# Kernel tuning notes

Measured on AMD Instinct MI355X. Metric: run time of the kernel, lower is better.

The kernel has to match this reference:

```python
import jax, jax.numpy as jnp
import numpy as np

B, L, H, V = 64, 2048, 1024, 50257


def setup_inputs() -> dict:
    key = jax.random.key(0)
    ks = jax.random.split(key, 12)
    s = 0.02
    return {
        "input_seq": jax.random.randint(ks[0], (B,), 0, V),
        "encoder_outputs": jax.random.normal(ks[1], (L, B, H), jnp.float32),
        "h0": jax.random.normal(ks[2], (1, B, H), jnp.float32),
        "c0": jax.random.normal(ks[3], (1, B, H), jnp.float32),
        "emb": jax.random.normal(ks[4], (V, H), jnp.float32) * s,
        "W_ih": jax.random.normal(ks[5], (4 * H, H), jnp.float32) * s,
        "W_hh": jax.random.normal(ks[6], (4 * H, H), jnp.float32) * s,
        "b_ih": jnp.zeros((4 * H,), jnp.float32),
        "b_hh": jnp.zeros((4 * H,), jnp.float32),
        "W_concat": jax.random.normal(ks[7], (H, 2 * H), jnp.float32) * s,
        "b_concat": jnp.zeros((H,), jnp.float32),
        "W_out": jax.random.normal(ks[8], (V, H), jnp.float32) * s,
        "b_out": jnp.zeros((V,), jnp.float32),
    }


def reference(input_seq, encoder_outputs, h0, c0, emb, W_ih, W_hh, b_ih, b_hh,
              W_concat, b_concat, W_out, b_out):
    # Embedding lookup (dropout is identity at eval)
    x = emb[input_seq]                      # [B, H]
    h, c = h0[0], c0[0]                     # [B, H] each (n_layers == 1)

    # Single LSTM step, PyTorch gate order (i, f, g, o)
    gates = x @ W_ih.T + b_ih + h @ W_hh.T + b_hh   # [B, 4H]
    i, f, g, o = jnp.split(gates, 4, axis=-1)
    i, f, o = jax.nn.sigmoid(i), jax.nn.sigmoid(f), jax.nn.sigmoid(o)
    g = jnp.tanh(g)
    c1 = f * c + i * g
    h1 = o * jnp.tanh(c1)                   # rnn_output, [B, H]

    # Luong 'dot' attention: replaces the per-(b,i) python double loop
    energies = jnp.einsum('bh,lbh->bl', h1, encoder_outputs)   # [B, L]
    attn = jax.nn.softmax(energies, axis=1)                    # [B, L]
    context = jnp.einsum('bl,lbh->bh', attn, encoder_outputs)  # [B, H]

    concat_out = jnp.tanh(jnp.concatenate([h1, context], axis=1) @ W_concat.T + b_concat)
    output = concat_out @ W_out.T + b_out                      # [B, V]

    return output, h1[None], c1[None], attn[:, None, :]
```

## Files before the change

kernel.cpp:

```cpp
#include <hip/hip_runtime.h>
#include <math.h>

#define B 64
#define Lw 2048
#define Hd 1024
#define Vd 50257

#define WS_CATB   0
#define WS_ENERGY 65536
#define WS_PART   196608
#define WS_CONC   2310144

#define OUT_H1   3216448
#define OUT_C1   3281984
#define OUT_ATTN 3347520

#define NCHUNK 32
#define LCHUNK 64
#define PSTRIDE 1032

typedef __bf16 bf16x8 __attribute__((ext_vector_type(8)));
typedef float f32x4 __attribute__((ext_vector_type(4)));

__device__ __forceinline__ float sigm(float x) { return 1.f / (1.f + expf(-x)); }

#define CVT8(dst, w0, w1)                                            \
    dst[0] = (__bf16)w0.x; dst[1] = (__bf16)w0.y;                    \
    dst[2] = (__bf16)w0.z; dst[3] = (__bf16)w0.w;                    \
    dst[4] = (__bf16)w1.x; dst[5] = (__bf16)w1.y;                    \
    dst[6] = (__bf16)w1.z; dst[7] = (__bf16)w1.w;

__global__ void k_gates_lstm(const int* __restrict__ seq,
                             const float* __restrict__ emb, const float* __restrict__ h0,
                             const float* __restrict__ W_ih, const float* __restrict__ W_hh,
                             const float* __restrict__ b_ih, const float* __restrict__ b_hh,
                             const float* __restrict__ c0,
                             float* __restrict__ h1o, float* __restrict__ c1o,
                             __bf16* __restrict__ catb)
{
    __shared__ float lds[8][64][20];
    __shared__ float gsum[16][66];

    int wave = threadIdx.x >> 6, lane = threadIdx.x & 63;
    int hh0 = blockIdx.x * 4;
    int rloc = lane & 15;
    int wrow = (rloc >> 2) * Hd + hh0 + (rloc & 3);
    int kq = lane >> 4;
    int isH = wave >> 2;
    int kbase = (wave & 3) * 256;

    const float* wp = (isH ? W_hh : W_ih) + (size_t)wrow * Hd + kbase + kq * 8;

    f32x4 acc[4] = {{0.f,0.f,0.f,0.f},{0.f,0.f,0.f,0.f},
                    {0.f,0.f,0.f,0.f},{0.f,0.f,0.f,0.f}};

    if (!isH) {
        int tok[4];
#pragma unroll
        for (int mt = 0; mt < 4; ++mt) tok[mt] = seq[mt * 16 + rloc];
#pragma unroll 2
        for (int k0 = 0; k0 < 256; k0 += 32) {
            float4 w0 = *(const float4*)(wp + k0);
            float4 w1 = *(const float4*)(wp + k0 + 4);
            bf16x8 bf; CVT8(bf, w0, w1);
#pragma unroll
            for (int mt = 0; mt < 4; ++mt) {
                const float* xp = emb + (size_t)tok[mt] * Hd + kbase + k0 + kq * 8;
                float4 a0 = *(const float4*)xp;
                float4 a1 = *(const float4*)(xp + 4);
                bf16x8 af; CVT8(af, a0, a1);
                acc[mt] = __builtin_amdgcn_mfma_f32_16x16x32_bf16(af, bf, acc[mt], 0, 0, 0);
            }
        }
    } else {
#pragma unroll 2
        for (int k0 = 0; k0 < 256; k0 += 32) {
            float4 w0 = *(const float4*)(wp + k0);
            float4 w1 = *(const float4*)(wp + k0 + 4);
            bf16x8 bhi, blo;
            {
                float wf[8] = {w0.x, w0.y, w0.z, w0.w, w1.x, w1.y, w1.z, w1.w};
#pragma unroll
                for (int i = 0; i < 8; ++i) {
                    __bf16 hi = (__bf16)wf[i];
                    bhi[i] = hi;
                    blo[i] = (__bf16)(wf[i] - (float)hi);
                }
            }
#pragma unroll
            for (int mt = 0; mt < 4; ++mt) {
                const float* hp = h0 + (size_t)(mt * 16 + rloc) * Hd + kbase + k0 + kq * 8;
                float4 a0 = *(const float4*)hp;
                float4 a1 = *(const float4*)(hp + 4);
                float hf[8] = {a0.x, a0.y, a0.z, a0.w, a1.x, a1.y, a1.z, a1.w};
                bf16x8 ahi, alo;
#pragma unroll
                for (int i = 0; i < 8; ++i) {
                    __bf16 hi = (__bf16)hf[i];
                    ahi[i] = hi;
                    alo[i] = (__bf16)(hf[i] - (float)hi);
                }
                acc[mt] = __builtin_amdgcn_mfma_f32_16x16x32_bf16(ahi, bhi, acc[mt], 0, 0, 0);
                acc[mt] = __builtin_amdgcn_mfma_f32_16x16x32_bf16(ahi, blo, acc[mt], 0, 0, 0);
                acc[mt] = __builtin_amdgcn_mfma_f32_16x16x32_bf16(alo, bhi, acc[mt], 0, 0, 0);
            }
        }
    }

#pragma unroll
    for (int mt = 0; mt < 4; ++mt)
        *(f32x4*)&lds[wave][lane][mt * 4] = acc[mt];
    __syncthreads();

    if (wave < 4) {
        int mt = wave;
        float bv = b_ih[wrow] + b_hh[wrow];
#pragma unroll
        for (int r = 0; r < 4; ++r) {
            float s = 0.f;
#pragma unroll
            for (int w = 0; w < 8; ++w) s += lds[w][lane][mt * 4 + r];
            int m = mt * 16 + kq * 4 + r;
            gsum[rloc][m] = s + bv;
        }
    }
    __syncthreads();

    int t = threadIdx.x;
    if (t < 256) {
        int b = t & 63, hl = t >> 6;
        int hh = hh0 + hl;
        float gi = gsum[0 + hl][b];
        float gf = gsum[4 + hl][b];
        float gg = gsum[8 + hl][b];
        float go = gsum[12 + hl][b];
        float c  = c0[(size_t)b * Hd + hh];
        float c1 = sigm(gf) * c + sigm(gi) * tanhf(gg);
        float h1 = sigm(go) * tanhf(c1);
        h1o[(size_t)b * Hd + hh] = h1;
        c1o[(size_t)b * Hd + hh] = c1;
        catb[(size_t)(hh >> 3) * 512 + b * 8 + (hh & 7)] = (__bf16)h1;
    }
}

__global__ void k_attn_part(const float* __restrict__ enc, const float* __restrict__ h1,
                            float* __restrict__ energy, float* __restrict__ part)
{
    int chunk = blockIdx.x, b = blockIdx.y;
    int wave = threadIdx.x >> 6, lane = threadIdx.x & 63;

    float4 qv[4], ctx[4];
#pragma unroll
    for (int q = 0; q < 4; ++q) {
        qv[q] = *(const float4*)(h1 + (size_t)b * Hd + q * 256 + lane * 4);
        ctx[q] = make_float4(0.f, 0.f, 0.f, 0.f);
    }
    float m = -INFINITY, s = 0.f;

    for (int i = 0; i < LCHUNK / 8; ++i) {
        int l = chunk * LCHUNK + i * 8 + wave * 2;
        const float* ep0 = enc + ((size_t)l * B + b) * Hd + lane * 4;
        const float* ep1 = ep0 + (size_t)B * Hd;
        float4 ev0[4], ev1[4];
#pragma unroll
        for (int q = 0; q < 4; ++q) {
            ev0[q] = *(const float4*)(ep0 + q * 256);
            ev1[q] = *(const float4*)(ep1 + q * 256);
        }
        float d0 = 0.f, d1 = 0.f;
#pragma unroll
        for (int q = 0; q < 4; ++q) {
            d0 += ev0[q].x * qv[q].x + ev0[q].y * qv[q].y
                + ev0[q].z * qv[q].z + ev0[q].w * qv[q].w;
            d1 += ev1[q].x * qv[q].x + ev1[q].y * qv[q].y
                + ev1[q].z * qv[q].z + ev1[q].w * qv[q].w;
        }
#pragma unroll
        for (int off = 32; off >= 1; off >>= 1) {
            d0 += __shfl_xor(d0, off);
            d1 += __shfl_xor(d1, off);
        }
        if (lane == 0) {
            energy[(size_t)b * Lw + l] = d0;
            energy[(size_t)b * Lw + l + 1] = d1;
        }

        float mn = fmaxf(d0, d1);
        if (mn > m) {
            float sc = expf(m - mn);
            s *= sc;
#pragma unroll
            for (int q = 0; q < 4; ++q) {
                ctx[q].x *= sc; ctx[q].y *= sc; ctx[q].z *= sc; ctx[q].w *= sc;
            }
            m = mn;
        }
        float w0 = expf(d0 - m), w1 = expf(d1 - m);
        s += w0 + w1;
#pragma unroll
        for (int q = 0; q < 4; ++q) {
            ctx[q].x += w0 * ev0[q].x + w1 * ev1[q].x;
            ctx[q].y += w0 * ev0[q].y + w1 * ev1[q].y;
            ctx[q].z += w0 * ev0[q].z + w1 * ev1[q].z;
            ctx[q].w += w0 * ev0[q].w + w1 * ev1[q].w;
        }
    }

    __shared__ float lctx[4][Hd];
    __shared__ float lms[4][2];
#pragma unroll
    for (int q = 0; q < 4; ++q)
        *(float4*)(&lctx[wave][q * 256 + lane * 4]) = ctx[q];
    if (lane == 0) { lms[wave][0] = m; lms[wave][1] = s; }
    __syncthreads();

    float mb = fmaxf(fmaxf(lms[0][0], lms[1][0]), fmaxf(lms[2][0], lms[3][0]));
    float sc0 = expf(lms[0][0] - mb), sc1 = expf(lms[1][0] - mb);
    float sc2 = expf(lms[2][0] - mb), sc3 = expf(lms[3][0] - mb);
    float sb = lms[0][1] * sc0 + lms[1][1] * sc1 + lms[2][1] * sc2 + lms[3][1] * sc3;

    int t = threadIdx.x;
    float* pb = part + (size_t)(chunk * B + b) * PSTRIDE;
    float4 a0 = *(float4*)(&lctx[0][t * 4]);
    float4 a1 = *(float4*)(&lctx[1][t * 4]);
    float4 a2 = *(float4*)(&lctx[2][t * 4]);
    float4 a3 = *(float4*)(&lctx[3][t * 4]);
    float4 v;
    v.x = a0.x * sc0 + a1.x * sc1 + a2.x * sc2 + a3.x * sc3;
    v.y = a0.y * sc0 + a1.y * sc1 + a2.y * sc2 + a3.y * sc3;
    v.z = a0.z * sc0 + a1.z * sc1 + a2.z * sc2 + a3.z * sc3;
    v.w = a0.w * sc0 + a1.w * sc1 + a2.w * sc2 + a3.w * sc3;
    *(float4*)(pb + t * 4) = v;
    if (t == 0) { pb[1024] = mb; pb[1025] = sb; }
}

__global__ void k_attn_combine(const float* __restrict__ part,
                               const float* __restrict__ energy,
                               __bf16* __restrict__ catb, float* __restrict__ attn)
{
    int b = blockIdx.x, t = threadIdx.x;
    float m = -INFINITY;
#pragma unroll
    for (int c = 0; c < NCHUNK; ++c)
        m = fmaxf(m, part[(size_t)(c * B + b) * PSTRIDE + 1024]);
    float s = 0.f, scl[NCHUNK];
#pragma unroll
    for (int c = 0; c < NCHUNK; ++c) {
        const float* pb = part + (size_t)(c * B + b) * PSTRIDE;
        scl[c] = expf(pb[1024] - m);
        s += pb[1025] * scl[c];
    }
    float4 v = make_float4(0.f, 0.f, 0.f, 0.f);
#pragma unroll
    for (int c = 0; c < NCHUNK; ++c) {
        float4 p = *(const float4*)(part + (size_t)(c * B + b) * PSTRIDE + t * 4);
        v.x += p.x * scl[c]; v.y += p.y * scl[c]; v.z += p.z * scl[c]; v.w += p.w * scl[c];
    }
    float inv = 1.f / s;
    v.x *= inv; v.y *= inv; v.z *= inv; v.w *= inv;
    int k = 1024 + t * 4;
    __bf16* cp = catb + (size_t)(k >> 3) * 512 + b * 8 + (k & 7);
    cp[0] = (__bf16)v.x; cp[1] = (__bf16)v.y;
    cp[2] = (__bf16)v.z; cp[3] = (__bf16)v.w;

#pragma unroll
    for (int j = 0; j < 8; ++j) {
        int l = t + j * 256;
        attn[(size_t)b * Lw + l] = expf(energy[(size_t)b * Lw + l] - m) * inv;
    }
}

__global__ void k_concat_mfma(const __bf16* __restrict__ catb,
                              const float* __restrict__ W, const float* __restrict__ bias,
                              __bf16* __restrict__ conc)
{
    __shared__ float lds[8][64][20];
    int wave = threadIdx.x >> 6, lane = threadIdx.x & 63;
    int n0 = blockIdx.x * 16;
    int nl = n0 + (lane & 15);
    int kq = lane >> 4;
    int kbase = wave * 256;

    const float* wp = W + (size_t)nl * (2 * Hd) + kbase + kq * 8;
    const __bf16* ap = catb + (lane & 15) * 8;

    f32x4 acc[4] = {{0.f,0.f,0.f,0.f},{0.f,0.f,0.f,0.f},
                    {0.f,0.f,0.f,0.f},{0.f,0.f,0.f,0.f}};

#pragma unroll 4
    for (int k0 = 0; k0 < 256; k0 += 32) {
        float4 w0 = *(const float4*)(wp + k0);
        float4 w1 = *(const float4*)(wp + k0 + 4);
        bf16x8 bf; CVT8(bf, w0, w1);
        int kb = ((kbase + k0) >> 3) + kq;
#pragma unroll
        for (int mt = 0; mt < 4; ++mt) {
            bf16x8 a = *(const bf16x8*)(ap + (size_t)kb * 512 + mt * 128);
            acc[mt] = __builtin_amdgcn_mfma_f32_16x16x32_bf16(a, bf, acc[mt], 0, 0, 0);
        }
    }

#pragma unroll
    for (int mt = 0; mt < 4; ++mt)
        *(f32x4*)&lds[wave][lane][mt * 4] = acc[mt];
    __syncthreads();

    if (wave < 4) {
        int mt = wave;
        float bv = bias[nl];
#pragma unroll
        for (int r = 0; r < 4; ++r) {
            float s = 0.f;
#pragma unroll
            for (int w = 0; w < 8; ++w) s += lds[w][lane][mt * 4 + r];
            int m = mt * 16 + kq * 4 + r;
            conc[(size_t)(nl >> 3) * 512 + m * 8 + (nl & 7)] = (__bf16)tanhf(s + bv);
        }
    }
}

__global__ void k_vocab_mfma(const __bf16* __restrict__ apack,
                             const float* __restrict__ W,
                             const float* __restrict__ bias,
                             float* __restrict__ out)
{
    int wave = threadIdx.x >> 6;
    int lane = threadIdx.x & 63;
    int n0 = (blockIdx.x * 2 + wave) * 16;
    if (n0 > Vd - 16) n0 = Vd - 16;

    int nl = n0 + (lane & 15);
    int kq = lane >> 4;
    const float* wp = W + (size_t)nl * Hd + kq * 8;
    const __bf16* ap = apack + (size_t)(lane & 15) * 8;

    f32x4 acc[4] = {{0.f,0.f,0.f,0.f},{0.f,0.f,0.f,0.f},
                    {0.f,0.f,0.f,0.f},{0.f,0.f,0.f,0.f}};

    float4 c0 = *(const float4*)(wp + 0);
    float4 c1 = *(const float4*)(wp + 4);
    float4 c2 = *(const float4*)(wp + 32);
    float4 c3 = *(const float4*)(wp + 36);

#pragma unroll 2
    for (int k0 = 0; k0 < Hd; k0 += 64) {
        int kn = (k0 + 64 < Hd) ? (k0 + 64) : k0;
        float4 p0 = *(const float4*)(wp + kn);
        float4 p1 = *(const float4*)(wp + kn + 4);
        float4 p2 = *(const float4*)(wp + kn + 32);
        float4 p3 = *(const float4*)(wp + kn + 36);

        bf16x8 bf0; CVT8(bf0, c0, c1);
        bf16x8 bf1; CVT8(bf1, c2, c3);
        int kb0 = (k0 >> 3) + kq, kb1 = kb0 + 4;
#pragma unroll
        for (int mt = 0; mt < 4; ++mt) {
            bf16x8 a0 = *(const bf16x8*)(ap + (size_t)kb0 * 512 + mt * 128);
            acc[mt] = __builtin_amdgcn_mfma_f32_16x16x32_bf16(a0, bf0, acc[mt], 0, 0, 0);
        }
#pragma unroll
        for (int mt = 0; mt < 4; ++mt) {
            bf16x8 a1 = *(const bf16x8*)(ap + (size_t)kb1 * 512 + mt * 128);
            acc[mt] = __builtin_amdgcn_mfma_f32_16x16x32_bf16(a1, bf1, acc[mt], 0, 0, 0);
        }
        c0 = p0; c1 = p1; c2 = p2; c3 = p3;
    }

    float bv = bias[nl];
#pragma unroll
    for (int mt = 0; mt < 4; ++mt)
#pragma unroll
        for (int r = 0; r < 4; ++r) {
            int m = mt * 16 + (lane >> 4) * 4 + r;
            out[(size_t)m * Vd + nl] = acc[mt][r] + bv;
        }
}

extern "C" void kernel_launch(void* const* d_in, const int* in_sizes, int n_in,
                              void* d_out, int out_size, void* d_ws, size_t ws_size,
                              hipStream_t stream)
{
    const int*   seq    = (const int*)d_in[0];
    const float* enc    = (const float*)d_in[1];
    const float* h0     = (const float*)d_in[2];
    const float* c0     = (const float*)d_in[3];
    const float* emb    = (const float*)d_in[4];
    const float* W_ih   = (const float*)d_in[5];
    const float* W_hh   = (const float*)d_in[6];
    const float* b_ih   = (const float*)d_in[7];
    const float* b_hh   = (const float*)d_in[8];
    const float* W_cat  = (const float*)d_in[9];
    const float* b_cat  = (const float*)d_in[10];
    const float* W_out  = (const float*)d_in[11];
    const float* b_out  = (const float*)d_in[12];
    float* out = (float*)d_out;
    float* ws  = (float*)d_ws;

    __bf16* catb   = (__bf16*)(ws + WS_CATB);
    float*  energy = ws + WS_ENERGY;
    float*  part   = ws + WS_PART;
    __bf16* conc   = (__bf16*)(ws + WS_CONC);

    k_gates_lstm<<<256, 512, 0, stream>>>(seq, emb, h0, W_ih, W_hh, b_ih, b_hh, c0,
                                          out + OUT_H1, out + OUT_C1, catb);
    k_attn_part<<<dim3(NCHUNK, B), 256, 0, stream>>>(enc, out + OUT_H1, energy, part);
    k_attn_combine<<<B, 256, 0, stream>>>(part, energy, catb, out + OUT_ATTN);
    k_concat_mfma<<<64, 512, 0, stream>>>(catb, W_cat, b_cat, conc);
    k_vocab_mfma<<<1571, 128, 0, stream>>>(conc, W_out, b_out, out);
}
```

Before: 228.5 us.

## Restructure attention partial kernel so each wave streams contiguous encoder rows

Each wave now handles two adjacent batch entries for a given sequence position, so a block reads 16 consecutive batch rows (64KB contiguous) per position, in place of strided rows for a single batch. The sequence is split into 128 chunks of 16 rather than 32 chunks of 64, and each wave writes its own partial, which removes the in-block LDS merge and the barrier. The cost is a much larger partial buffer (128 partials per batch row), more work in the combine kernel, and a loop there that is no longer unrolled.

```diff
diff --git a/kernel.cpp b/kernel.cpp
--- a/kernel.cpp
+++ b/kernel.cpp
@@ -6,18 +6,19 @@
 #define Hd 1024
 #define Vd 50257
 
+#define LCB 16
+#define NLCHUNK (Lw / LCB)
+#define BGRP 16
+#define PSTRIDE 1032
+
 #define WS_CATB   0
 #define WS_ENERGY 65536
 #define WS_PART   196608
-#define WS_CONC   2310144
+#define WS_CONC   8650752
 
 #define OUT_H1   3216448
 #define OUT_C1   3281984
 #define OUT_ATTN 3347520
-
-#define NCHUNK 32
-#define LCHUNK 64
-#define PSTRIDE 1032
 
 typedef __bf16 bf16x8 __attribute__((ext_vector_type(8)));
 typedef float f32x4 __attribute__((ext_vector_type(4)));
@@ -143,37 +144,42 @@
     }
 }
 
-__global__ void k_attn_part(const float* __restrict__ enc, const float* __restrict__ h1,
-                            float* __restrict__ energy, float* __restrict__ part)
-{
-    int chunk = blockIdx.x, b = blockIdx.y;
+__global__ void __launch_bounds__(512, 4)
+k_attn_part(const float* __restrict__ enc, const float* __restrict__ h1,
+            float* __restrict__ energy, float* __restrict__ part)
+{
+    int lc = blockIdx.x, bg = blockIdx.y;
     int wave = threadIdx.x >> 6, lane = threadIdx.x & 63;
-
-    float4 qv[4], ctx[4];
+    int b0 = bg * BGRP + wave * 2;
+    int b1 = b0 + 1;
+
+    float4 qv0[4], qv1[4], ctx0[4], ctx1[4];
 #pragma unroll
     for (int q = 0; q < 4; ++q) {
-        qv[q] = *(const float4*)(h1 + (size_t)b * Hd + q * 256 + lane * 4);
-        ctx[q] = make_float4(0.f, 0.f, 0.f, 0.f);
-    }
-    float m = -INFINITY, s = 0.f;
-
-    for (int i = 0; i < LCHUNK / 8; ++i) {
-        int l = chunk * LCHUNK + i * 8 + wave * 2;
-        const float* ep0 = enc + ((size_t)l * B + b) * Hd + lane * 4;
-        const float* ep1 = ep0 + (size_t)B * Hd;
+        qv0[q] = *(const float4*)(h1 + (size_t)b0 * Hd + q * 256 + lane * 4);
+        qv1[q] = *(const float4*)(h1 + (size_t)b1 * Hd + q * 256 + lane * 4);
+        ctx0[q] = make_float4(0.f, 0.f, 0.f, 0.f);
+        ctx1[q] = make_float4(0.f, 0.f, 0.f, 0.f);
+    }
+    float m0 = -INFINITY, s0 = 0.f, m1 = -INFINITY, s1 = 0.f;
+
+    for (int i = 0; i < LCB; ++i) {
+        int l = lc * LCB + i;
+        const float* e0 = enc + ((size_t)l * B + b0) * Hd + lane * 4;
+        const float* e1 = e0 + Hd;
         float4 ev0[4], ev1[4];
 #pragma unroll
         for (int q = 0; q < 4; ++q) {
-            ev0[q] = *(const float4*)(ep0 + q * 256);
-            ev1[q] = *(const float4*)(ep1 + q * 256);
+            ev0[q] = *(const float4*)(e0 + q * 256);
+            ev1[q] = *(const float4*)(e1 + q * 256);
         }
         float d0 = 0.f, d1 = 0.f;
 #pragma unroll
         for (int q = 0; q < 4; ++q) {
-            d0 += ev0[q].x * qv[q].x + ev0[q].y * qv[q].y
-                + ev0[q].z * qv[q].z + ev0[q].w * qv[q].w;
-            d1 += ev1[q].x * qv[q].x + ev1[q].y * qv[q].y
-                + ev1[q].z * qv[q].z + ev1[q].w * qv[q].w;
+            d0 += ev0[q].x * qv0[q].x + ev0[q].y * qv0[q].y
+                + ev0[q].z * qv0[q].z + ev0[q].w * qv0[q].w;
+            d1 += ev1[q].x * qv1[q].x + ev1[q].y * qv1[q].y
+                + ev1[q].z * qv1[q].z + ev1[q].w * qv1[q].w;
         }
 #pragma unroll
         for (int off = 32; off >= 1; off >>= 1) {
@@ -181,57 +187,56 @@
             d1 += __shfl_xor(d1, off);
         }
         if (lane == 0) {
-            energy[(size_t)b * Lw + l] = d0;
-            energy[(size_t)b * Lw + l + 1] = d1;
-        }
-
-        float mn = fmaxf(d0, d1);
-        if (mn > m) {
-            float sc = expf(m - mn);
-            s *= sc;
+            energy[(size_t)b0 * Lw + l] = d0;
+            energy[(size_t)b1 * Lw + l] = d1;
+        }
+
+        if (d0 > m0) {
+            float sc = expf(m0 - d0);
+            s0 *= sc;
 #pragma unroll
             for (int q = 0; q < 4; ++q) {
-                ctx[q].x *= sc; ctx[q].y *= sc; ctx[q].z *= sc; ctx[q].w *= sc;
+                ctx0[q].x *= sc; ctx0[q].y *= sc; ctx0[q].z *= sc; ctx0[q].w *= sc;
             }
-            m = mn;
-        }
-        float w0 = expf(d0 - m), w1 = expf(d1 - m);
-        s += w0 + w1;
+            m0 = d0;
+        }
+        float w0 = expf(d0 - m0);
+        s0 += w0;
 #pragma unroll
         for (int q = 0; q < 4; ++q) {
-            ctx[q].x += w0 * ev0[q].x + w1 * ev1[q].x;
-            ctx[q].y += w0 * ev0[q].y + w1 * ev1[q].y;
-            ctx[q].z += w0 * ev0[q].z + w1 * ev1[q].z;
-            ctx[q].w += w0 * ev0[q].w + w1 * ev1[q].w;
-        }
-    }
-
-    __shared__ float lctx[4][Hd];
-    __shared__ float lms[4][2];
-#pragma unroll
-    for (int q = 0; q < 4; ++q)
-        *(float4*)(&lctx[wave][q * 256 + lane * 4]) = ctx[q];
-    if (lane == 0) { lms[wave][0] = m; lms[wave][1] = s; }
-    __syncthreads();
-
-    float mb = fmaxf(fmaxf(lms[0][0], lms[1][0]), fmaxf(lms[2][0], lms[3][0]));
-    float sc0 = expf(lms[0][0] - mb), sc1 = expf(lms[1][0] - mb);
-    float sc2 = expf(lms[2][0] - mb), sc3 = expf(lms[3][0] - mb);
-    float sb = lms[0][1] * sc0 + lms[1][1] * sc1 + lms[2][1] * sc2 + lms[3][1] * sc3;
-
-    int t = threadIdx.x;
-    float* pb = part + (size_t)(chunk * B + b) * PSTRIDE;
-    float4 a0 = *(float4*)(&lctx[0][t * 4]);
-    float4 a1 = *(float4*)(&lctx[1][t * 4]);
-    float4 a2 = *(float4*)(&lctx[2][t * 4]);
-    float4 a3 = *(float4*)(&lctx[3][t * 4]);
-    float4 v;
-    v.x = a0.x * sc0 + a1.x * sc1 + a2.x * sc2 + a3.x * sc3;
-    v.y = a0.y * sc0 + a1.y * sc1 + a2.y * sc2 + a3.y * sc3;
-    v.z = a0.z * sc0 + a1.z * sc1 + a2.z * sc2 + a3.z * sc3;
-    v.w = a0.w * sc0 + a1.w * sc1 + a2.w * sc2 + a3.w * sc3;
-    *(float4*)(pb + t * 4) = v;
-    if (t == 0) { pb[1024] = mb; pb[1025] = sb; }
+            ctx0[q].x += w0 * ev0[q].x; ctx0[q].y += w0 * ev0[q].y;
+            ctx0[q].z += w0 * ev0[q].z; ctx0[q].w += w0 * ev0[q].w;
+        }
+
+        if (d1 > m1) {
+            float sc = expf(m1 - d1);
+            s1 *= sc;
+#pragma unroll
+            for (int q = 0; q < 4; ++q) {
+                ctx1[q].x *= sc; ctx1[q].y *= sc; ctx1[q].z *= sc; ctx1[q].w *= sc;
+            }
+            m1 = d1;
+        }
+        float w1 = expf(d1 - m1);
+        s1 += w1;
+#pragma unroll
+        for (int q = 0; q < 4; ++q) {
+            ctx1[q].x += w1 * ev1[q].x; ctx1[q].y += w1 * ev1[q].y;
+            ctx1[q].z += w1 * ev1[q].z; ctx1[q].w += w1 * ev1[q].w;
+        }
+    }
+
+    float* pb0 = part + ((size_t)lc * B + b0) * PSTRIDE;
+    float* pb1 = part + ((size_t)lc * B + b1) * PSTRIDE;
+#pragma unroll
+    for (int q = 0; q < 4; ++q) {
+        *(float4*)(pb0 + q * 256 + lane * 4) = ctx0[q];
+        *(float4*)(pb1 + q * 256 + lane * 4) = ctx1[q];
+    }
+    if (lane == 0) {
+        pb0[1024] = m0; pb0[1025] = s0;
+        pb1[1024] = m1; pb1[1025] = s1;
+    }
 }
 
 __global__ void k_attn_combine(const float* __restrict__ part,
@@ -240,21 +245,16 @@
 {
     int b = blockIdx.x, t = threadIdx.x;
     float m = -INFINITY;
-#pragma unroll
-    for (int c = 0; c < NCHUNK; ++c)
-        m = fmaxf(m, part[(size_t)(c * B + b) * PSTRIDE + 1024]);
-    float s = 0.f, scl[NCHUNK];
-#pragma unroll
-    for (int c = 0; c < NCHUNK; ++c) {
-        const float* pb = part + (size_t)(c * B + b) * PSTRIDE;
-        scl[c] = expf(pb[1024] - m);
-        s += pb[1025] * scl[c];
-    }
+    for (int c = 0; c < NLCHUNK; ++c)
+        m = fmaxf(m, part[((size_t)c * B + b) * PSTRIDE + 1024]);
+    float s = 0.f;
     float4 v = make_float4(0.f, 0.f, 0.f, 0.f);
-#pragma unroll
-    for (int c = 0; c < NCHUNK; ++c) {
-        float4 p = *(const float4*)(part + (size_t)(c * B + b) * PSTRIDE + t * 4);
-        v.x += p.x * scl[c]; v.y += p.y * scl[c]; v.z += p.z * scl[c]; v.w += p.w * scl[c];
+    for (int c = 0; c < NLCHUNK; ++c) {
+        const float* pb = part + ((size_t)c * B + b) * PSTRIDE;
+        float scl = expf(pb[1024] - m);
+        s += pb[1025] * scl;
+        float4 p = *(const float4*)(pb + t * 4);
+        v.x += p.x * scl; v.y += p.y * scl; v.z += p.z * scl; v.w += p.w * scl;
     }
     float inv = 1.f / s;
     v.x *= inv; v.y *= inv; v.z *= inv; v.w *= inv;
@@ -403,7 +403,8 @@
 
     k_gates_lstm<<<256, 512, 0, stream>>>(seq, emb, h0, W_ih, W_hh, b_ih, b_hh, c0,
                                           out + OUT_H1, out + OUT_C1, catb);
-    k_attn_part<<<dim3(NCHUNK, B), 256, 0, stream>>>(enc, out + OUT_H1, energy, part);
+    k_attn_part<<<dim3(NLCHUNK, B / BGRP), 512, 0, stream>>>(enc, out + OUT_H1,
+                                                             energy, part);
     k_attn_combine<<<B, 256, 0, stream>>>(part, energy, catb, out + OUT_ATTN);
     k_concat_mfma<<<64, 512, 0, stream>>>(catb, W_cat, b_cat, conc);
     k_vocab_mfma<<<1571, 128, 0, stream>>>(conc, W_out, b_out, out);
```

Result: slower. 259.1 us (+13.4%).
